# Performance work log

Measured on AMD Instinct MI355X. Metric: run time of the kernel, lower is better.

The kernel has to match this reference:

```python
import jax, jax.numpy as jnp
import numpy as np

N_NODES = 100000
N_EDGES = 1600000
HIDDEN = 128
LAYERS = 2


def setup_inputs() -> dict:
    key = jax.random.key(0)
    k1, k2, k3, k4 = jax.random.split(key, 4)
    x = jax.random.normal(k1, (N_NODES, HIDDEN), dtype=jnp.float32)
    edge_index = jax.random.randint(k2, (2, N_EDGES), 0, N_NODES, dtype=jnp.int32)
    # Glorot-ish init for per-layer GCN weights, small bias
    Ws = jax.random.normal(k3, (LAYERS, HIDDEN, HIDDEN), dtype=jnp.float32) / np.sqrt(HIDDEN).astype(np.float32)
    bs = jax.random.normal(k4, (LAYERS, HIDDEN), dtype=jnp.float32) * 0.01
    return {"x": x, "edge_index": edge_index, "Ws": Ws, "bs": bs}


def reference(x, edge_index, Ws, bs):
    # PyG GCNConv with normalize=True, add_self_loops=False:
    #   x' = D^{-1/2} A D^{-1/2} (x W) + b,  deg = in-degree at target (col) nodes
    src = edge_index[0]  # message sources (row)
    dst = edge_index[1]  # message targets (col), aggregation index
    ones = jnp.ones(src.shape[0], dtype=x.dtype)
    deg = jax.ops.segment_sum(ones, dst, num_segments=N_NODES)
    dinv = jnp.where(deg > 0, jax.lax.rsqrt(jnp.maximum(deg, 1.0)), jnp.zeros_like(deg))
    norm = dinv[src] * dinv[dst]  # [E] symmetric edge normalization
    for l in range(Ws.shape[0]):
        h = x @ Ws[l]                                  # [N, D] dense transform
        msg = h[src] * norm[:, None]                   # [E, D] gather + scale
        x = jax.ops.segment_sum(msg, dst, num_segments=N_NODES) + bs[l]
    return x
```

## Files before the change

### kernel.cpp

```cpp
#include <hip/hip_runtime.h>

#define HID 128
#define WFRAG (HID*HID)

typedef __attribute__((ext_vector_type(8))) short bf16x8;
typedef __attribute__((ext_vector_type(4))) float f32x4;

static __device__ __forceinline__ unsigned short f2bf(float f){
  unsigned u = __float_as_uint(f);
  unsigned r = (u + 0x7FFF + ((u >> 16) & 1)) >> 16;
  return (unsigned short)r;
}
static __device__ __forceinline__ float bf2f_lo(unsigned u){ return __uint_as_float(u << 16); }
static __device__ __forceinline__ float bf2f_hi(unsigned u){ return __uint_as_float(u & 0xFFFF0000u); }

static __device__ __forceinline__ unsigned cvtpk(float lo, float hi){
  unsigned r;
  asm volatile("v_cvt_pk_bf16_f32 %0, %1, %2" : "=v"(r) : "v"(lo), "v"(hi));
  return r;
}

__global__ __launch_bounds__(256) void k_pos(const int* __restrict__ dst, int* __restrict__ fill,
                                             int* __restrict__ pos, int E){
  int e = blockIdx.x*256 + threadIdx.x;
  if (e < E) pos[e] = atomicAdd(&fill[dst[e]], 1);
}

__global__ __launch_bounds__(256) void k_bsum(const int* __restrict__ deg, int* __restrict__ bsum, int N){
  __shared__ int sm[256];
  int t = threadIdx.x, n = blockIdx.x*256 + t;
  sm[t] = (n < N) ? deg[n] : 0;
  __syncthreads();
  for (int off = 128; off > 0; off >>= 1){
    if (t < off) sm[t] += sm[t+off];
    __syncthreads();
  }
  if (t == 0) bsum[blockIdx.x] = sm[0];
}

__global__ __launch_bounds__(512) void k_scan1(const int* __restrict__ bsum, int* __restrict__ bbase, int nb){
  __shared__ int sm[512];
  int t = threadIdx.x;
  int v = (t < nb) ? bsum[t] : 0;
  sm[t] = v;
  __syncthreads();
  for (int off = 1; off < 512; off <<= 1){
    int u = (t >= off) ? sm[t-off] : 0;
    __syncthreads();
    sm[t] += u;
    __syncthreads();
  }
  if (t < nb) bbase[t] = sm[t] - v;
}

__global__ __launch_bounds__(256) void k_rowstart(const int* __restrict__ deg, const int* __restrict__ bbase,
                                                  int* __restrict__ rowstart, float* __restrict__ dinv, int N){
  __shared__ int sm[256];
  int t = threadIdx.x, n = blockIdx.x*256 + t;
  int d = (n < N) ? deg[n] : 0;
  sm[t] = d;
  __syncthreads();
  for (int off = 1; off < 256; off <<= 1){
    int v = (t >= off) ? sm[t-off] : 0;
    __syncthreads();
    sm[t] += v;
    __syncthreads();
  }
  if (n < N){
    rowstart[n] = bbase[blockIdx.x] + sm[t] - d;
    dinv[n] = d > 0 ? rsqrtf((float)d) : 0.0f;
  }
}

__global__ __launch_bounds__(256) void k_scatter(const int* __restrict__ src, const int* __restrict__ dst,
                                                 const int* __restrict__ pos, const int* __restrict__ rowstart,
                                                 int* __restrict__ slots, int E){
  int i0 = (blockIdx.x*256 + threadIdx.x)*2;
  if (i0 + 1 < E){
    int2 s = *(const int2*)(src + i0);
    int2 d = *(const int2*)(dst + i0);
    int2 p = *(const int2*)(pos + i0);
    slots[rowstart[d.x] + p.x] = s.x;
    slots[rowstart[d.y] + p.y] = s.y;
  } else if (i0 < E){
    slots[rowstart[dst[i0]] + pos[i0]] = src[i0];
  }
}

__global__ __launch_bounds__(256) void k_wprep(const float* __restrict__ Ws, unsigned short* __restrict__ Whi,
                                               unsigned short* __restrict__ Wlo){
  int layer = blockIdx.x;
  const float* W = Ws + (size_t)layer*HID*HID;
  for (int idx = threadIdx.x; idx < 2048; idx += 256){
    int lane = idx & 63, kstep = (idx>>6)&3, nblk = idx>>8;
    int col = 16*nblk + (lane&15);
    int k0  = 32*kstep + 8*(lane>>4);
    size_t obase = ((size_t)(layer*8 + nblk)*4 + kstep)*512 + (size_t)lane*8;
    for (int j = 0; j < 8; j++){
      float v = W[(size_t)(k0+j)*HID + col];
      unsigned short h = f2bf(v);
      float hf = __uint_as_float((unsigned)h << 16);
      Whi[obase+j] = h;
      Wlo[obase+j] = f2bf(v - hf);
    }
  }
}

__global__ __launch_bounds__(256) void k_gemm_mfma(const float* __restrict__ X, const unsigned short* __restrict__ Whi,
                                                   const unsigned short* __restrict__ Wlo,
                                                   const float* __restrict__ dinv,
                                                   unsigned short* __restrict__ H2u, int N){
  int t = threadIdx.x, w = t>>6, l = t&63;
  int row0 = blockIdx.x*32;
  int lrow = l & 15, lk = (l>>4)*8;
  f32x4 acc[2][2] = {};
#pragma unroll 1
  for (int kstep = 0; kstep < 4; kstep++){
    bf16x8 ahi[2], alo[2];
#pragma unroll
    for (int m = 0; m < 2; m++){
      int row = row0 + 16*m + lrow;
      if (row >= N) row = N-1;
      const float* ap = X + (size_t)row*HID + kstep*32 + lk;
      float4 a0 = *(const float4*)ap;
      float4 a1 = *(const float4*)(ap+4);
      int4 hh, ll;
      hh.x = cvtpk(a0.x, a0.y); hh.y = cvtpk(a0.z, a0.w);
      hh.z = cvtpk(a1.x, a1.y); hh.w = cvtpk(a1.z, a1.w);
      ll.x = cvtpk(a0.x - bf2f_lo(hh.x), a0.y - bf2f_hi(hh.x));
      ll.y = cvtpk(a0.z - bf2f_lo(hh.y), a0.w - bf2f_hi(hh.y));
      ll.z = cvtpk(a1.x - bf2f_lo(hh.z), a1.y - bf2f_hi(hh.z));
      ll.w = cvtpk(a1.z - bf2f_lo(hh.w), a1.w - bf2f_hi(hh.w));
      ahi[m] = *(bf16x8*)&hh;
      alo[m] = *(bf16x8*)&ll;
    }
    bf16x8 bhi[2], blo[2];
#pragma unroll
    for (int n = 0; n < 2; n++){
      size_t base = ((size_t)((2*w+n)*4 + kstep))*512 + (size_t)l*8;
      bhi[n] = *(const bf16x8*)(Whi + base);
      blo[n] = *(const bf16x8*)(Wlo + base);
    }
#pragma unroll
    for (int m = 0; m < 2; m++)
#pragma unroll
      for (int n = 0; n < 2; n++){
        acc[m][n] = __builtin_amdgcn_mfma_f32_16x16x32_bf16(ahi[m], bhi[n], acc[m][n], 0, 0, 0);
        acc[m][n] = __builtin_amdgcn_mfma_f32_16x16x32_bf16(alo[m], bhi[n], acc[m][n], 0, 0, 0);
        acc[m][n] = __builtin_amdgcn_mfma_f32_16x16x32_bf16(ahi[m], blo[n], acc[m][n], 0, 0, 0);
      }
  }
#pragma unroll
  for (int m = 0; m < 2; m++)
#pragma unroll
    for (int r = 0; r < 4; r++){
      int row = row0 + 16*m + 4*(l>>4) + r;
      if (row < N){
        float dv = dinv[row];
#pragma unroll
        for (int n = 0; n < 2; n++){
          int col = 16*(2*w+n) + lrow;
          H2u[(size_t)row*HID + col] = f2bf(dv * acc[m][n][r]);
        }
      }
    }
}

__global__ __launch_bounds__(256) void k_agg(const uint4* __restrict__ H4, const int* __restrict__ slots,
                                             const int* __restrict__ rowstart, const int* __restrict__ deg,
                                             const float* __restrict__ dinv,
                                             const float* __restrict__ bias, float* __restrict__ out, int N){
  int wid = threadIdx.x >> 6, lane = threadIdx.x & 63;
  int n = blockIdx.x*4 + wid;
  if (n >= N) return;
  int st = rowstart[n], cnt = deg[n];
  int g = lane >> 4, c = lane & 15;
  float a[8] = {0.f,0.f,0.f,0.f,0.f,0.f,0.f,0.f};
  for (int j = 0; j < cnt; j += 8){
    int j0 = j + g, j1 = j + 4 + g;
    int cl = cnt - 1;
    int i0 = slots[st + (j0 < cnt ? j0 : cl)];
    int i1 = slots[st + (j1 < cnt ? j1 : cl)];
    uint4 v0 = H4[(size_t)i0*16 + c];
    uint4 v1 = H4[(size_t)i1*16 + c];
    if (j0 >= cnt){ v0.x=0u; v0.y=0u; v0.z=0u; v0.w=0u; }
    if (j1 >= cnt){ v1.x=0u; v1.y=0u; v1.z=0u; v1.w=0u; }
    a[0] += bf2f_lo(v0.x) + bf2f_lo(v1.x);
    a[1] += bf2f_hi(v0.x) + bf2f_hi(v1.x);
    a[2] += bf2f_lo(v0.y) + bf2f_lo(v1.y);
    a[3] += bf2f_hi(v0.y) + bf2f_hi(v1.y);
    a[4] += bf2f_lo(v0.z) + bf2f_lo(v1.z);
    a[5] += bf2f_hi(v0.z) + bf2f_hi(v1.z);
    a[6] += bf2f_lo(v0.w) + bf2f_lo(v1.w);
    a[7] += bf2f_hi(v0.w) + bf2f_hi(v1.w);
  }
#pragma unroll
  for (int q = 0; q < 8; q++){
    a[q] += __shfl_xor(a[q], 16);
    a[q] += __shfl_xor(a[q], 32);
  }
  if (g == 0){
    float dv = dinv[n];
    const float4* b4 = (const float4*)bias;
    float4 b0 = b4[c*2], b1 = b4[c*2+1];
    float4 o0 = make_float4(dv*a[0]+b0.x, dv*a[1]+b0.y, dv*a[2]+b0.z, dv*a[3]+b0.w);
    float4 o1 = make_float4(dv*a[4]+b1.x, dv*a[5]+b1.y, dv*a[6]+b1.z, dv*a[7]+b1.w);
    float4* orow = (float4*)(out + (size_t)n*HID);
    orow[c*2]   = o0;
    orow[c*2+1] = o1;
  }
}

extern "C" void kernel_launch(void* const* d_in, const int* in_sizes, int n_in,
                              void* d_out, int out_size, void* d_ws, size_t ws_size,
                              hipStream_t stream){
  const float* x  = (const float*)d_in[0];
  const int*   ei = (const int*)d_in[1];
  const float* Ws = (const float*)d_in[2];
  const float* bs = (const float*)d_in[3];
  const int N = in_sizes[0] / HID;
  const int E = in_sizes[1] / 2;
  const int L = in_sizes[2] / (HID*HID);
  const int* src = ei;
  const int* dst = ei + E;
  const int NB = (N + 255)/256;

  char* w = (char*)d_ws;
  int*   fill     = (int*)w;   w += (size_t)N*4;
  size_t zbytes = (size_t)(w - (char*)d_ws);
  int*   bsum     = (int*)w;   w += (size_t)NB*4;
  int*   bbase    = (int*)w;   w += (size_t)NB*4;
  float* dinv     = (float*)w; w += (size_t)N*4;
  int*   rowstart = (int*)w;   w += (size_t)N*4;
  int*   pos      = (int*)w;   w += (size_t)E*4;
  int*   slots    = (int*)w;   w += (size_t)E*4 + 64;
  unsigned short* h2u = (unsigned short*)w; w += (size_t)N*HID*2;
  unsigned short* whi = (unsigned short*)w; w += (size_t)L*WFRAG*2;
  unsigned short* wlo = (unsigned short*)w; w += (size_t)L*WFRAG*2;

  hipMemsetAsync(d_ws, 0, zbytes, stream);

  int gE  = (E + 255)/256;
  int gE2 = (E/2 + 255)/256 + 1;
  k_pos     <<<gE, 256, 0, stream>>>(dst, fill, pos, E);
  k_bsum    <<<NB, 256, 0, stream>>>(fill, bsum, N);
  k_scan1   <<<1, 512, 0, stream>>>(bsum, bbase, NB);
  k_rowstart<<<NB, 256, 0, stream>>>(fill, bbase, rowstart, dinv, N);
  k_wprep   <<<L,  256, 0, stream>>>(Ws, whi, wlo);
  k_scatter <<<gE2, 256, 0, stream>>>(src, dst, pos, rowstart, slots, E);

  const float* xin = x;
  float* out = (float*)d_out;
  for (int l = 0; l < L; l++){
    k_gemm_mfma<<<(N + 31)/32, 256, 0, stream>>>(xin, whi + (size_t)l*WFRAG, wlo + (size_t)l*WFRAG,
                                                 dinv, h2u, N);
    k_agg<<<(N + 3)/4, 256, 0, stream>>>((const uint4*)h2u, slots, rowstart, fill,
                                         dinv, bs + (size_t)l*HID, out, N);
    xin = out;
  }
}
```

Baseline: 350.5 us.

## Fuse CSR build kernels, use atomic block allocation, deepen aggregation gather

Merges the weight preparation into the edge-position kernel and the first-layer GEMM into the slot-scatter kernel by splitting each grid by block index. The three-kernel scan is replaced by one kernel in which each block reserves its row range with an atomicAdd on a global cursor. Rows are therefore no longer in node order in the slots array, which is still correct because each row keeps its own start. The aggregation loop now issues four independent gathers per iteration instead of two, so more memory requests are in flight. The aim is fewer launches, less serialization between small kernels, and better latency hiding in the gather.

```diff
diff --git a/kernel.cpp b/kernel.cpp
--- a/kernel.cpp
+++ b/kernel.cpp
@@ -20,76 +20,9 @@
   return r;
 }
 
-__global__ __launch_bounds__(256) void k_pos(const int* __restrict__ dst, int* __restrict__ fill,
-                                             int* __restrict__ pos, int E){
-  int e = blockIdx.x*256 + threadIdx.x;
-  if (e < E) pos[e] = atomicAdd(&fill[dst[e]], 1);
-}
-
-__global__ __launch_bounds__(256) void k_bsum(const int* __restrict__ deg, int* __restrict__ bsum, int N){
-  __shared__ int sm[256];
-  int t = threadIdx.x, n = blockIdx.x*256 + t;
-  sm[t] = (n < N) ? deg[n] : 0;
-  __syncthreads();
-  for (int off = 128; off > 0; off >>= 1){
-    if (t < off) sm[t] += sm[t+off];
-    __syncthreads();
-  }
-  if (t == 0) bsum[blockIdx.x] = sm[0];
-}
-
-__global__ __launch_bounds__(512) void k_scan1(const int* __restrict__ bsum, int* __restrict__ bbase, int nb){
-  __shared__ int sm[512];
-  int t = threadIdx.x;
-  int v = (t < nb) ? bsum[t] : 0;
-  sm[t] = v;
-  __syncthreads();
-  for (int off = 1; off < 512; off <<= 1){
-    int u = (t >= off) ? sm[t-off] : 0;
-    __syncthreads();
-    sm[t] += u;
-    __syncthreads();
-  }
-  if (t < nb) bbase[t] = sm[t] - v;
-}
-
-__global__ __launch_bounds__(256) void k_rowstart(const int* __restrict__ deg, const int* __restrict__ bbase,
-                                                  int* __restrict__ rowstart, float* __restrict__ dinv, int N){
-  __shared__ int sm[256];
-  int t = threadIdx.x, n = blockIdx.x*256 + t;
-  int d = (n < N) ? deg[n] : 0;
-  sm[t] = d;
-  __syncthreads();
-  for (int off = 1; off < 256; off <<= 1){
-    int v = (t >= off) ? sm[t-off] : 0;
-    __syncthreads();
-    sm[t] += v;
-    __syncthreads();
-  }
-  if (n < N){
-    rowstart[n] = bbase[blockIdx.x] + sm[t] - d;
-    dinv[n] = d > 0 ? rsqrtf((float)d) : 0.0f;
-  }
-}
-
-__global__ __launch_bounds__(256) void k_scatter(const int* __restrict__ src, const int* __restrict__ dst,
-                                                 const int* __restrict__ pos, const int* __restrict__ rowstart,
-                                                 int* __restrict__ slots, int E){
-  int i0 = (blockIdx.x*256 + threadIdx.x)*2;
-  if (i0 + 1 < E){
-    int2 s = *(const int2*)(src + i0);
-    int2 d = *(const int2*)(dst + i0);
-    int2 p = *(const int2*)(pos + i0);
-    slots[rowstart[d.x] + p.x] = s.x;
-    slots[rowstart[d.y] + p.y] = s.y;
-  } else if (i0 < E){
-    slots[rowstart[dst[i0]] + pos[i0]] = src[i0];
-  }
-}
-
-__global__ __launch_bounds__(256) void k_wprep(const float* __restrict__ Ws, unsigned short* __restrict__ Whi,
-                                               unsigned short* __restrict__ Wlo){
-  int layer = blockIdx.x;
+static __device__ __forceinline__ void wprep_body(int layer, const float* __restrict__ Ws,
+                                                  unsigned short* __restrict__ Whi,
+                                                  unsigned short* __restrict__ Wlo){
   const float* W = Ws + (size_t)layer*HID*HID;
   for (int idx = threadIdx.x; idx < 2048; idx += 256){
     int lane = idx & 63, kstep = (idx>>6)&3, nblk = idx>>8;
@@ -106,12 +39,47 @@
   }
 }
 
-__global__ __launch_bounds__(256) void k_gemm_mfma(const float* __restrict__ X, const unsigned short* __restrict__ Whi,
-                                                   const unsigned short* __restrict__ Wlo,
-                                                   const float* __restrict__ dinv,
-                                                   unsigned short* __restrict__ H2u, int N){
+__global__ __launch_bounds__(256) void k_pos_wprep(const int* __restrict__ dst, int* __restrict__ fill,
+                                                   int* __restrict__ pos, int E, int L,
+                                                   const float* __restrict__ Ws,
+                                                   unsigned short* __restrict__ Whi,
+                                                   unsigned short* __restrict__ Wlo){
+  int bid = blockIdx.x;
+  if (bid < L){ wprep_body(bid, Ws, Whi, Wlo); return; }
+  int e = (bid - L)*256 + threadIdx.x;
+  if (e < E) pos[e] = atomicAdd(&fill[dst[e]], 1);
+}
+
+__global__ __launch_bounds__(256) void k_alloc(const int* __restrict__ deg, int* __restrict__ rowstart,
+                                               float* __restrict__ dinv, int* __restrict__ cursor, int N){
+  __shared__ int sm[256];
+  __shared__ int sbase;
+  int t = threadIdx.x;
+  int n = blockIdx.x*256 + t;
+  int d = (n < N) ? deg[n] : 0;
+  sm[t] = d;
+  __syncthreads();
+  for (int off = 1; off < 256; off <<= 1){
+    int v = (t >= off) ? sm[t-off] : 0;
+    __syncthreads();
+    sm[t] += v;
+    __syncthreads();
+  }
+  if (t == 255) sbase = atomicAdd(cursor, sm[255]);
+  __syncthreads();
+  if (n < N){
+    rowstart[n] = sbase + sm[t] - d;
+    dinv[n] = d > 0 ? rsqrtf((float)d) : 0.0f;
+  }
+}
+
+static __device__ __forceinline__ void gemm_body(int bid, const float* __restrict__ X,
+                                                 const unsigned short* __restrict__ Whi,
+                                                 const unsigned short* __restrict__ Wlo,
+                                                 const float* __restrict__ dinv,
+                                                 unsigned short* __restrict__ H2u, int N){
   int t = threadIdx.x, w = t>>6, l = t&63;
-  int row0 = blockIdx.x*32;
+  int row0 = bid*32;
   int lrow = l & 15, lk = (l>>4)*8;
   f32x4 acc[2][2] = {};
 #pragma unroll 1
@@ -166,6 +134,36 @@
     }
 }
 
+__global__ __launch_bounds__(256) void k_gemm_scatter(const float* __restrict__ X,
+                                                      const unsigned short* __restrict__ Whi,
+                                                      const unsigned short* __restrict__ Wlo,
+                                                      const float* __restrict__ dinv,
+                                                      unsigned short* __restrict__ H2u, int N, int Gg,
+                                                      const int* __restrict__ src, const int* __restrict__ dst,
+                                                      const int* __restrict__ pos, const int* __restrict__ rowstart,
+                                                      int* __restrict__ slots, int E){
+  int bid = blockIdx.x;
+  if (bid < Gg){ gemm_body(bid, X, Whi, Wlo, dinv, H2u, N); return; }
+  int i0 = ((bid - Gg)*256 + threadIdx.x)*2;
+  if (i0 + 1 < E){
+    int2 s = *(const int2*)(src + i0);
+    int2 d = *(const int2*)(dst + i0);
+    int2 p = *(const int2*)(pos + i0);
+    slots[rowstart[d.x] + p.x] = s.x;
+    slots[rowstart[d.y] + p.y] = s.y;
+  } else if (i0 < E){
+    slots[rowstart[dst[i0]] + pos[i0]] = src[i0];
+  }
+}
+
+__global__ __launch_bounds__(256) void k_gemm_mfma(const float* __restrict__ X,
+                                                   const unsigned short* __restrict__ Whi,
+                                                   const unsigned short* __restrict__ Wlo,
+                                                   const float* __restrict__ dinv,
+                                                   unsigned short* __restrict__ H2u, int N){
+  gemm_body(blockIdx.x, X, Whi, Wlo, dinv, H2u, N);
+}
+
 __global__ __launch_bounds__(256) void k_agg(const uint4* __restrict__ H4, const int* __restrict__ slots,
                                              const int* __restrict__ rowstart, const int* __restrict__ deg,
                                              const float* __restrict__ dinv,
@@ -176,23 +174,29 @@
   int st = rowstart[n], cnt = deg[n];
   int g = lane >> 4, c = lane & 15;
   float a[8] = {0.f,0.f,0.f,0.f,0.f,0.f,0.f,0.f};
-  for (int j = 0; j < cnt; j += 8){
-    int j0 = j + g, j1 = j + 4 + g;
+  for (int j = 0; j < cnt; j += 16){
     int cl = cnt - 1;
-    int i0 = slots[st + (j0 < cnt ? j0 : cl)];
-    int i1 = slots[st + (j1 < cnt ? j1 : cl)];
-    uint4 v0 = H4[(size_t)i0*16 + c];
-    uint4 v1 = H4[(size_t)i1*16 + c];
-    if (j0 >= cnt){ v0.x=0u; v0.y=0u; v0.z=0u; v0.w=0u; }
-    if (j1 >= cnt){ v1.x=0u; v1.y=0u; v1.z=0u; v1.w=0u; }
-    a[0] += bf2f_lo(v0.x) + bf2f_lo(v1.x);
-    a[1] += bf2f_hi(v0.x) + bf2f_hi(v1.x);
-    a[2] += bf2f_lo(v0.y) + bf2f_lo(v1.y);
-    a[3] += bf2f_hi(v0.y) + bf2f_hi(v1.y);
-    a[4] += bf2f_lo(v0.z) + bf2f_lo(v1.z);
-    a[5] += bf2f_hi(v0.z) + bf2f_hi(v1.z);
-    a[6] += bf2f_lo(v0.w) + bf2f_lo(v1.w);
-    a[7] += bf2f_hi(v0.w) + bf2f_hi(v1.w);
+    int ix[4];
+#pragma unroll
+    for (int q = 0; q < 4; q++){
+      int jj = j + 4*q + g;
+      ix[q] = slots[st + (jj < cnt ? jj : cl)];
+    }
+    uint4 v[4];
+#pragma unroll
+    for (int q = 0; q < 4; q++) v[q] = H4[(size_t)ix[q]*16 + c];
+#pragma unroll
+    for (int q = 0; q < 4; q++){
+      if (j + 4*q + g >= cnt){ v[q].x=0u; v[q].y=0u; v[q].z=0u; v[q].w=0u; }
+      a[0] += bf2f_lo(v[q].x);
+      a[1] += bf2f_hi(v[q].x);
+      a[2] += bf2f_lo(v[q].y);
+      a[3] += bf2f_hi(v[q].y);
+      a[4] += bf2f_lo(v[q].z);
+      a[5] += bf2f_hi(v[q].z);
+      a[6] += bf2f_lo(v[q].w);
+      a[7] += bf2f_hi(v[q].w);
+    }
   }
 #pragma unroll
   for (int q = 0; q < 8; q++){
@@ -227,9 +231,8 @@
 
   char* w = (char*)d_ws;
   int*   fill     = (int*)w;   w += (size_t)N*4;
+  int*   cursor   = (int*)w;   w += 16;
   size_t zbytes = (size_t)(w - (char*)d_ws);
-  int*   bsum     = (int*)w;   w += (size_t)NB*4;
-  int*   bbase    = (int*)w;   w += (size_t)NB*4;
   float* dinv     = (float*)w; w += (size_t)N*4;
   int*   rowstart = (int*)w;   w += (size_t)N*4;
   int*   pos      = (int*)w;   w += (size_t)E*4;
@@ -241,21 +244,19 @@
   hipMemsetAsync(d_ws, 0, zbytes, stream);
 
   int gE  = (E + 255)/256;
-  int gE2 = (E/2 + 255)/256 + 1;
-  k_pos     <<<gE, 256, 0, stream>>>(dst, fill, pos, E);
-  k_bsum    <<<NB, 256, 0, stream>>>(fill, bsum, N);
-  k_scan1   <<<1, 512, 0, stream>>>(bsum, bbase, NB);
-  k_rowstart<<<NB, 256, 0, stream>>>(fill, bbase, rowstart, dinv, N);
-  k_wprep   <<<L,  256, 0, stream>>>(Ws, whi, wlo);
-  k_scatter <<<gE2, 256, 0, stream>>>(src, dst, pos, rowstart, slots, E);
-
-  const float* xin = x;
+  int Gs  = (E/2 + 255)/256 + 1;
+  int Gg  = (N + 31)/32;
+  k_pos_wprep<<<gE + L, 256, 0, stream>>>(dst, fill, pos, E, L, Ws, whi, wlo);
+  k_alloc    <<<NB, 256, 0, stream>>>(fill, rowstart, dinv, cursor, N);
+  k_gemm_scatter<<<Gg + Gs, 256, 0, stream>>>(x, whi, wlo, dinv, h2u, N, Gg,
+                                              src, dst, pos, rowstart, slots, E);
   float* out = (float*)d_out;
-  for (int l = 0; l < L; l++){
-    k_gemm_mfma<<<(N + 31)/32, 256, 0, stream>>>(xin, whi + (size_t)l*WFRAG, wlo + (size_t)l*WFRAG,
-                                                 dinv, h2u, N);
+  k_agg<<<(N + 3)/4, 256, 0, stream>>>((const uint4*)h2u, slots, rowstart, fill,
+                                       dinv, bs, out, N);
+  for (int l = 1; l < L; l++){
+    k_gemm_mfma<<<Gg, 256, 0, stream>>>(out, whi + (size_t)l*WFRAG, wlo + (size_t)l*WFRAG,
+                                        dinv, h2u, N);
     k_agg<<<(N + 3)/4, 256, 0, stream>>>((const uint4*)h2u, slots, rowstart, fill,
                                          dinv, bs + (size_t)l*HID, out, N);
-    xin = out;
-  }
-}
+  }
+}
```

New measurement: 332.9 us. 5.0% less time.
